# Performance work log

Measured on AMD Instinct MI355X. Metric: run time of the kernel, lower is better.

## Reference

```python
import jax, jax.numpy as jnp
import numpy as np

EPS = 1e-5
NUM_HEAD = 8
HEAD_DIM = 64
SCALE = HEAD_DIM ** -0.5


def setup_inputs() -> dict:
    key = jax.random.key(0)
    ks = jax.random.split(key, 3)
    b, n, dim = 4, 2048, 512
    inner = NUM_HEAD * HEAD_DIM  # 512
    x = jax.random.normal(ks[0], (b, n, dim), dtype=jnp.float32)
    ln_w = jnp.ones((dim,), jnp.float32)
    ln_b = jnp.zeros((dim,), jnp.float32)
    qkv_w = jax.random.normal(ks[1], (3 * inner, dim), jnp.float32) * (dim ** -0.5)
    qkv_b = jnp.zeros((3 * inner,), jnp.float32)
    out_w = jax.random.normal(ks[2], (dim, inner), jnp.float32) * (inner ** -0.5)
    out_b = jnp.zeros((dim,), jnp.float32)
    return {"x": x, "ln_w": ln_w, "ln_b": ln_b, "qkv_w": qkv_w,
            "qkv_b": qkv_b, "out_w": out_w, "out_b": out_b}


def reference(x, ln_w, ln_b, qkv_w, qkv_b, out_w, out_b):
    b, n, dim = x.shape
    # Pre-norm LayerNorm
    mu = jnp.mean(x, axis=-1, keepdims=True)
    var = jnp.mean(jnp.square(x - mu), axis=-1, keepdims=True)
    xn = (x - mu) * jax.lax.rsqrt(var + EPS) * ln_w + ln_b
    # QKV projection (torch Linear: y = x @ W.T + b)
    qkv = xn @ qkv_w.T + qkv_b  # [b, n, 3*inner]
    q, k, v = jnp.split(qkv, 3, axis=-1)
    def heads(t):  # [b, n, inner] -> [b, h, n, d]
        return t.reshape(b, n, NUM_HEAD, HEAD_DIM).transpose(0, 2, 1, 3)
    q, k, v = heads(q), heads(k), heads(v)
    # Naive full attention (materializes [b, h, n, n])
    dots = jnp.einsum('bhqd,bhkd->bhqk', q, k) * SCALE
    attn = jax.nn.softmax(dots, axis=-1)
    o = jnp.einsum('bhqk,bhkd->bhqd', attn, v)
    o = o.transpose(0, 2, 1, 3).reshape(b, n, NUM_HEAD * HEAD_DIM)
    return o @ out_w.T + out_b
```

## Files before the change

kernel.cpp:

```cpp
#include <hip/hip_runtime.h>

typedef __attribute__((ext_vector_type(8))) short bf16x8;
typedef __attribute__((ext_vector_type(4))) float floatx4;
typedef __attribute__((ext_vector_type(16))) float floatx16;
typedef __attribute__((ext_vector_type(4))) unsigned int uintx4;

#define B_    4
#define N_    2048
#define DIM_  512
#define NH_   8
#define HD_   64
#define SCALE_ 0.125f
#define SL2E_ (0.125f * 1.44269504f)

__device__ __forceinline__ unsigned short f32_to_bf16(float f) {
    return (unsigned short)((__float_as_uint(f) + 0x8000u) >> 16);
}

__device__ __forceinline__ float bf16_to_f32(unsigned short u) {
    return __uint_as_float(((unsigned int)u) << 16);
}

__device__ __forceinline__ floatx4 mfma16(bf16x8 a, bf16x8 b, floatx4 c) {
    return __builtin_amdgcn_mfma_f32_16x16x32_bf16(a, b, c, 0, 0, 0);
}

__device__ __forceinline__ floatx16 mfma32(bf16x8 a, bf16x8 b, floatx16 c) {
    return __builtin_amdgcn_mfma_f32_32x32x16_bf16(a, b, c, 0, 0, 0);
}

__device__ __forceinline__ floatx4 fzero4() {
    floatx4 z = {0.f, 0.f, 0.f, 0.f};
    return z;
}

__device__ __forceinline__ floatx16 fzero16() {
    floatx16 z;
#pragma unroll
    for (int i = 0; i < 16; i++) z[i] = 0.f;
    return z;
}

__device__ __forceinline__ unsigned int cvt_pk_bf16(float lo, float hi) {
    unsigned int r;
    asm("v_cvt_pk_bf16_f32 %0, %1, %2" : "=v"(r) : "v"(lo), "v"(hi));
    return r;
}

__device__ __forceinline__ void async16(const unsigned short* g, unsigned short* l) {
    __builtin_amdgcn_global_load_lds((const __attribute__((address_space(1))) void*)g,
                                     (__attribute__((address_space(3))) void*)l,
                                     16, 0, 0);
}

__global__ __launch_bounds__(256) void ln_cvt_kernel(const float* __restrict__ x,
                                                     const float* __restrict__ w,
                                                     const float* __restrict__ b,
                                                     unsigned short* __restrict__ xn,
                                                     const float* __restrict__ srcA,
                                                     const float* __restrict__ srcB,
                                                     unsigned short* __restrict__ dstA,
                                                     unsigned short* __restrict__ dstB) {
    const int NWQ = 3 * DIM_ * DIM_;
    if (blockIdx.x < 2048) {
        int wv = threadIdx.x >> 6;
        int lane = threadIdx.x & 63;
        int row = blockIdx.x * 4 + wv;
        const float4* xr = (const float4*)(x + (size_t)row * DIM_);
        float4 v0 = xr[lane * 2];
        float4 v1 = xr[lane * 2 + 1];
        float s  = (v0.x + v0.y + v0.z + v0.w) + (v1.x + v1.y + v1.z + v1.w);
        float sq = v0.x*v0.x + v0.y*v0.y + v0.z*v0.z + v0.w*v0.w +
                   v1.x*v1.x + v1.y*v1.y + v1.z*v1.z + v1.w*v1.w;
#pragma unroll
        for (int off = 1; off < 64; off <<= 1) {
            s  += __shfl_xor(s, off, 64);
            sq += __shfl_xor(sq, off, 64);
        }
        float mu   = s * (1.f / DIM_);
        float var  = sq * (1.f / DIM_) - mu * mu;
        float rstd = rsqrtf(var + 1e-5f);
        float4 w0 = ((const float4*)w)[lane * 2];
        float4 w1 = ((const float4*)w)[lane * 2 + 1];
        float4 b0 = ((const float4*)b)[lane * 2];
        float4 b1 = ((const float4*)b)[lane * 2 + 1];
        float y[8];
        y[0] = (v0.x - mu) * rstd * w0.x + b0.x;
        y[1] = (v0.y - mu) * rstd * w0.y + b0.y;
        y[2] = (v0.z - mu) * rstd * w0.z + b0.z;
        y[3] = (v0.w - mu) * rstd * w0.w + b0.w;
        y[4] = (v1.x - mu) * rstd * w1.x + b1.x;
        y[5] = (v1.y - mu) * rstd * w1.y + b1.y;
        y[6] = (v1.z - mu) * rstd * w1.z + b1.z;
        y[7] = (v1.w - mu) * rstd * w1.w + b1.w;
        uint4 pk;
        pk.x = (unsigned int)f32_to_bf16(y[0]) | ((unsigned int)f32_to_bf16(y[1]) << 16);
        pk.y = (unsigned int)f32_to_bf16(y[2]) | ((unsigned int)f32_to_bf16(y[3]) << 16);
        pk.z = (unsigned int)f32_to_bf16(y[4]) | ((unsigned int)f32_to_bf16(y[5]) << 16);
        pk.w = (unsigned int)f32_to_bf16(y[6]) | ((unsigned int)f32_to_bf16(y[7]) << 16);
        ((uint4*)(xn + (size_t)row * DIM_))[lane] = pk;
    } else {
        int e0 = ((blockIdx.x - 2048) * 256 + threadIdx.x) * 8;
        const float* src;
        unsigned short* dst;
        if (e0 < NWQ) { src = srcA + e0; dst = dstA + e0; }
        else          { src = srcB + (e0 - NWQ); dst = dstB + (e0 - NWQ); }
        float4 u0 = ((const float4*)src)[0];
        float4 u1 = ((const float4*)src)[1];
        uint4 pk;
        pk.x = (unsigned int)f32_to_bf16(u0.x) | ((unsigned int)f32_to_bf16(u0.y) << 16);
        pk.y = (unsigned int)f32_to_bf16(u0.z) | ((unsigned int)f32_to_bf16(u0.w) << 16);
        pk.z = (unsigned int)f32_to_bf16(u1.x) | ((unsigned int)f32_to_bf16(u1.y) << 16);
        pk.w = (unsigned int)f32_to_bf16(u1.z) | ((unsigned int)f32_to_bf16(u1.w) << 16);
        *(uint4*)dst = pk;
    }
}

#define GEMM_CORE512(A_, B_ptr, am0, bn0)                                           \
    __shared__ unsigned short Alds[2][128][32];                                     \
    __shared__ unsigned short Blds[2][128][32];                                     \
    int tid = threadIdx.x, lane = tid & 63, wid = tid >> 6;                         \
    int l15 = lane & 15, quad = lane >> 4;                                          \
    int wmloc = (wid >> 1) * 32, wnloc = (wid & 1) * 64;                            \
    int sr = lane >> 2;                                                             \
    int sc = (lane & 3) * 8;                                                        \
    int srow0 = 16 * wid;                                                           \
    floatx4 acc[2][4];                                                              \
    _Pragma("unroll")                                                               \
    for (int i = 0; i < 2; i++)                                                     \
        _Pragma("unroll")                                                           \
        for (int j = 0; j < 4; j++) acc[i][j] = fzero4();                           \
    int buf = 0;                                                                    \
    async16(A_ + (size_t)(am0 + srow0 + sr) * DIM_ + sc, &Alds[0][srow0][0]);       \
    async16(B_ptr + (size_t)(bn0 + srow0 + sr) * DIM_ + sc, &Blds[0][srow0][0]);    \
    __syncthreads();                                                                \
    for (int t = 0; t < 16; t++) {                                                  \
        if (t < 15) {                                                               \
            int k0 = (t + 1) * 32;                                                  \
            async16(A_ + (size_t)(am0 + srow0 + sr) * DIM_ + k0 + sc,               \
                    &Alds[buf ^ 1][srow0][0]);                                      \
            async16(B_ptr + (size_t)(bn0 + srow0 + sr) * DIM_ + k0 + sc,            \
                    &Blds[buf ^ 1][srow0][0]);                                      \
        }                                                                           \
        bf16x8 av[2], bv[4];                                                        \
        _Pragma("unroll")                                                           \
        for (int i = 0; i < 2; i++)                                                 \
            av[i] = *(const bf16x8*)(&Alds[buf][wmloc + 16 * i + l15][quad * 8]);   \
        _Pragma("unroll")                                                           \
        for (int j = 0; j < 4; j++)                                                 \
            bv[j] = *(const bf16x8*)(&Blds[buf][wnloc + 16 * j + l15][quad * 8]);   \
        _Pragma("unroll")                                                           \
        for (int i = 0; i < 2; i++)                                                 \
            _Pragma("unroll")                                                       \
            for (int j = 0; j < 4; j++)                                             \
                acc[i][j] = mfma16(av[i], bv[j], acc[i][j]);                        \
        __syncthreads();                                                            \
        buf ^= 1;                                                                   \
    }

__global__ __launch_bounds__(512, 6) void qkv_gemm(const unsigned short* __restrict__ A,
                                                   const unsigned short* __restrict__ Bw,
                                                   const float* __restrict__ bias,
                                                   unsigned short* __restrict__ Qh,
                                                   unsigned short* __restrict__ Kh,
                                                   unsigned short* __restrict__ Vt) {
    int am0 = blockIdx.x * 128, bn0 = blockIdx.y * 128;
    GEMM_CORE512(A, Bw, am0, bn0)

    if (bn0 >= 1024) {
        unsigned short* sc_ = &Alds[0][0][0] + wid * (16 * 40);
        int m0 = am0 + wmloc;
        int bidx = m0 >> 11;
        int t0 = m0 & 2047;
#pragma unroll
        for (int j = 0; j < 4; j++) {
            float bias_n = bias[bn0 + wnloc + 16 * j + l15];
#pragma unroll
            for (int i = 0; i < 2; i++)
#pragma unroll
                for (int r = 0; r < 4; r++)
                    sc_[l15 * 40 + 16 * i + quad * 4 + r] =
                        f32_to_bf16(acc[i][j][r] + bias_n);
            int nr = lane >> 2;
            int rem = (bn0 - 1024) + wnloc + 16 * j + nr;
            int head = rem >> 6, d = rem & 63;
            bf16x8 vv = *(const bf16x8*)(sc_ + nr * 40 + (lane & 3) * 8);
            *(bf16x8*)(Vt + ((size_t)(bidx * NH_ + head) * HD_ + d) * N_ +
                       t0 + (lane & 3) * 8) = vv;
        }
    } else {
#pragma unroll
        for (int i = 0; i < 2; i++) {
#pragma unroll
            for (int j = 0; j < 4; j++) {
                int n = bn0 + wnloc + 16 * j + l15;
                float bias_n = bias[n];
                int which = n >> 9;
                int rem = n & 511;
                int head = rem >> 6;
                int d = rem & 63;
#pragma unroll
                for (int r = 0; r < 4; r++) {
                    int m = am0 + wmloc + 16 * i + quad * 4 + r;
                    int b = m >> 11;
                    int t = m & 2047;
                    float val = acc[i][j][r] + bias_n;
                    if (which == 0) {
                        Qh[((size_t)(b * NH_ + head) * N_ + t) * HD_ + d] =
                            f32_to_bf16(val * SL2E_);
                    } else {
                        Kh[((size_t)(b * NH_ + head) * N_ + t) * HD_ + d] =
                            f32_to_bf16(val);
                    }
                }
            }
        }
    }
}

__global__ __launch_bounds__(256, 4) void out_gemm_fused(const unsigned short* __restrict__ Opart,
                                                         const float* __restrict__ lpart,
                                                         const unsigned short* __restrict__ Bw,
                                                         const float* __restrict__ bias,
                                                         float* __restrict__ out) {
    __shared__ unsigned short Alds[2][64][36];
    __shared__ unsigned short Blds[2][128][32];
    int tid = threadIdx.x, lane = tid & 63, wid = tid >> 6;
    int l15 = lane & 15, quad = lane >> 4;
    int wmloc = (wid >> 1) * 32, wnloc = (wid & 1) * 64;
    int am0 = blockIdx.x * 64, bn0 = blockIdx.y * 128;

    int arow = tid >> 2;
    int ac8 = (tid & 3) * 8;
    int token = am0 + arow;
    int bb = token >> 11;
    const size_t LSTR = (size_t)B_ * NH_ * N_;
    const size_t OSTR = (size_t)B_ * N_ * DIM_;
    const unsigned short* arow0 = Opart + (size_t)token * DIM_;
    const unsigned short* arow1 = arow0 + OSTR;

    int sr = lane >> 2;
    int sc = (lane & 3) * 8;

    floatx4 acc[2][4];
#pragma unroll
    for (int i = 0; i < 2; i++)
#pragma unroll
        for (int j = 0; j < 4; j++) acc[i][j] = fzero4();

#define STAGE_A(BUF, T)                                                         \
    {                                                                           \
        int k0 = (T) * 32;                                                      \
        int head = k0 >> 6;                                                     \
        size_t li = (size_t)(bb * NH_ + head) * N_ + (token & 2047);            \
        float l1 = lpart[li];                                                   \
        float l2 = lpart[LSTR + li];                                            \
        float inv = 1.f / (l1 + l2);                                            \
        float w1 = l1 * inv, w2 = l2 * inv;                                     \
        bf16x8 o0 = *(const bf16x8*)(arow0 + k0 + ac8);                         \
        bf16x8 o1 = *(const bf16x8*)(arow1 + k0 + ac8);                         \
        bf16x8 pk;                                                              \
        _Pragma("unroll")                                                       \
        for (int e = 0; e < 8; e++)                                             \
            pk[e] = (short)f32_to_bf16(                                         \
                w1 * bf16_to_f32((unsigned short)o0[e]) +                       \
                w2 * bf16_to_f32((unsigned short)o1[e]));                       \
        *(bf16x8*)(&Alds[BUF][arow][ac8]) = pk;                                 \
    }

#define STAGE_B(BUF, T)                                                         \
    {                                                                           \
        int k0 = (T) * 32;                                                      \
        _Pragma("unroll")                                                       \
        for (int i = 0; i < 2; i++) {                                           \
            int r0 = 32 * wid + 16 * i;                                         \
            async16(Bw + (size_t)(bn0 + r0 + sr) * DIM_ + k0 + sc,              \
                    &Blds[BUF][r0][0]);                                         \
        }                                                                       \
    }

    STAGE_B(0, 0)
    STAGE_A(0, 0)
    __syncthreads();
    int buf = 0;
    for (int t = 0; t < 16; t++) {
        if (t < 15) {
            STAGE_B(buf ^ 1, t + 1)
            STAGE_A(buf ^ 1, t + 1)
        }
        bf16x8 av[2], bv[4];
#pragma unroll
        for (int i = 0; i < 2; i++)
            av[i] = *(const bf16x8*)(&Alds[buf][wmloc + 16 * i + l15][quad * 8]);
#pragma unroll
        for (int j = 0; j < 4; j++)
            bv[j] = *(const bf16x8*)(&Blds[buf][wnloc + 16 * j + l15][quad * 8]);
#pragma unroll
        for (int i = 0; i < 2; i++)
#pragma unroll
            for (int j = 0; j < 4; j++)
                acc[i][j] = mfma16(av[i], bv[j], acc[i][j]);
        __syncthreads();
        buf ^= 1;
    }
#undef STAGE_A
#undef STAGE_B

#pragma unroll
    for (int i = 0; i < 2; i++) {
#pragma unroll
        for (int j = 0; j < 4; j++) {
            int n = bn0 + wnloc + 16 * j + l15;
            float bias_n = bias[n];
#pragma unroll
            for (int r = 0; r < 4; r++) {
                int m = am0 + wmloc + 16 * i + quad * 4 + r;
                out[(size_t)m * DIM_ + n] = acc[i][j][r] + bias_n;
            }
        }
    }
}

__global__ __launch_bounds__(512, 4) void attn_kernel(const unsigned short* __restrict__ Qh,
                                                      const unsigned short* __restrict__ Kh,
                                                      const unsigned short* __restrict__ Vtg,
                                                      unsigned short* __restrict__ Opart,
                                                      float* __restrict__ lpart) {
    int bh = blockIdx.y;
    int b = bh >> 3, head = bh & 7;
    int qt = blockIdx.x;
    int split = blockIdx.z;
    int kv0 = split << 10;
    int tid = threadIdx.x, lane = tid & 63, w = tid >> 6;
    int l31 = lane & 31, hi = lane >> 5;
    int xr = l31 & 7;

    const unsigned short* Qp = Qh + (size_t)bh * N_ * HD_;
    const unsigned short* Kg = Kh + (size_t)bh * N_ * HD_;
    const unsigned short* Vg = Vtg + (size_t)bh * HD_ * N_;

    int q0 = qt * 256 + w * 32;

    bf16x8 aQ[4];
    {
        const unsigned short* qrow = Qp + (size_t)(q0 + l31) * HD_ + hi * 8;
#pragma unroll
        for (int t = 0; t < 4; t++)
            aQ[t] = *(const bf16x8*)(qrow + 16 * t);
    }

    __shared__ unsigned short KV[4][2][64][64];
    __shared__ float l_sm[8][32];

    int srow = lane >> 3;
    int scol = ((lane & 7) ^ srow) * 8;

    const char* ptc[4];
#pragma unroll
    for (int t = 0; t < 4; t++)
        ptc[t] = (const char*)&KV[0][0][l31][(((2 * t + hi) ^ xr) * 8)];

    const unsigned short* kSrc = Kg + (size_t)(kv0 + 8 * w + srow) * HD_ + scol;
    const unsigned short* vSrc = Vg + (size_t)(8 * w + srow) * N_ + kv0 + scol;

#define STAGE_KV(BUF, IT)                                                       \
    {                                                                           \
        async16(kSrc + (size_t)(IT) * 64 * HD_, &KV[BUF][0][8 * w][0]);         \
        async16(vSrc + (size_t)(IT) * 64, &KV[BUF][1][8 * w][0]);               \
    }

#define VMW(N)  asm volatile("s_waitcnt vmcnt(" #N ")" ::: "memory")
#define RBAR()  asm volatile("s_barrier" ::: "memory")

    floatx16 of[2];
    of[0] = fzero16();
    of[1] = fzero16();
    float lsA = 0.f, lsB = 0.f;

#define COMPUTE(BUF)                                                            \
    {                                                                           \
        bf16x8 pa[4];                                                           \
        _Pragma("unroll")                                                       \
        for (int tau = 0; tau < 2; tau++) {                                     \
            bf16x8 kf[4];                                                       \
            _Pragma("unroll")                                                   \
            for (int t = 0; t < 4; t++)                                         \
                kf[t] = *(const bf16x8*)(ptc[t] + (BUF) * 16384 + tau * 4096);  \
            floatx16 acc = fzero16();                                           \
            __builtin_amdgcn_s_setprio(1);                                      \
            _Pragma("unroll")                                                   \
            for (int t = 0; t < 4; t++)                                         \
                acc = mfma32(kf[t], aQ[t], acc);                                \
            __builtin_amdgcn_s_setprio(0);                                      \
            float p[16];                                                        \
            _Pragma("unroll")                                                   \
            for (int r = 0; r < 16; r += 2) {                                   \
                p[r]     = __builtin_amdgcn_exp2f(acc[r]);                      \
                p[r + 1] = __builtin_amdgcn_exp2f(acc[r + 1]);                  \
                lsA += p[r];                                                    \
                lsB += p[r + 1];                                                \
            }                                                                   \
            unsigned int a0 = cvt_pk_bf16(p[0], p[1]);                          \
            unsigned int b0 = cvt_pk_bf16(p[4], p[5]);                          \
            unsigned int a1 = cvt_pk_bf16(p[2], p[3]);                          \
            unsigned int b1 = cvt_pk_bf16(p[6], p[7]);                          \
            unsigned int a2 = cvt_pk_bf16(p[8], p[9]);                          \
            unsigned int b2 = cvt_pk_bf16(p[12], p[13]);                        \
            unsigned int a3 = cvt_pk_bf16(p[10], p[11]);                        \
            unsigned int b3 = cvt_pk_bf16(p[14], p[15]);                        \
            asm("v_permlane32_swap_b32 %0, %1" : "+v"(a0), "+v"(b0));           \
            asm("v_permlane32_swap_b32 %0, %1" : "+v"(a1), "+v"(b1));           \
            asm("v_permlane32_swap_b32 %0, %1" : "+v"(a2), "+v"(b2));           \
            asm("v_permlane32_swap_b32 %0, %1" : "+v"(a3), "+v"(b3));           \
            uintx4 f0 = {a0, a1, b0, b1};                                       \
            uintx4 f1 = {a2, a3, b2, b3};                                       \
            pa[2 * tau]     = __builtin_bit_cast(bf16x8, f0);                   \
            pa[2 * tau + 1] = __builtin_bit_cast(bf16x8, f1);                   \
        }                                                                       \
        __builtin_amdgcn_s_setprio(1);                                          \
        _Pragma("unroll")                                                       \
        for (int s = 0; s < 4; s++) {                                           \
            _Pragma("unroll")                                                   \
            for (int dt = 0; dt < 2; dt++) {                                    \
                bf16x8 vf = *(const bf16x8*)(ptc[s] + (BUF) * 16384 + 8192 +    \
                                             dt * 4096);                        \
                of[dt] = mfma32(pa[s], vf, of[dt]);                             \
            }                                                                   \
        }                                                                       \
        __builtin_amdgcn_s_setprio(0);                                          \
    }

#define ITER(BUF, VN, SBUF, STILE, DOSTAGE)                                     \
    VMW(VN);                                                                    \
    RBAR();                                                                     \
    __builtin_amdgcn_sched_barrier(0);                                          \
    COMPUTE(BUF)                                                                \
    RBAR();                                                                     \
    if (DOSTAGE) STAGE_KV(SBUF, STILE)

    STAGE_KV(0, 0)
    STAGE_KV(1, 1)
    STAGE_KV(2, 2)

    for (int g = 0; g < 3; g++) {
        int base = g * 4;
        ITER(0, 4, 3, base + 3, 1);
        ITER(1, 4, 0, base + 4, 1);
        ITER(2, 4, 1, base + 5, 1);
        ITER(3, 4, 2, base + 6, 1);
    }
    ITER(0, 4, 3, 15, 1);
    ITER(1, 4, 0, 0, 0);
    ITER(2, 2, 0, 0, 0);
    ITER(3, 0, 0, 0, 0);
#undef ITER
#undef STAGE_KV
#undef COMPUTE
#undef VMW
#undef RBAR

    float lsum = lsA + lsB;
    lsum += __shfl_xor(lsum, 32, 64);
    if (hi == 0) {
        l_sm[w][l31] = __builtin_amdgcn_rcpf(lsum);
        lpart[(size_t)split * B_ * NH_ * N_ + (size_t)bh * N_ + q0 + l31] = lsum;
    }
    asm volatile("s_waitcnt lgkmcnt(0)" ::: "memory");

    unsigned short* Od = Opart + (size_t)split * B_ * N_ * DIM_;
#pragma unroll
    for (int r = 0; r < 16; r++) {
        int qr = (r & 3) + 8 * (r >> 2) + 4 * hi;
        float inv = l_sm[w][qr];
        int token = q0 + qr;
        size_t base = ((size_t)b * N_ + token) * DIM_ + (size_t)head * HD_;
#pragma unroll
        for (int dt = 0; dt < 2; dt++)
            Od[base + 32 * dt + l31] = f32_to_bf16(of[dt][r] * inv);
    }
}

extern "C" void kernel_launch(void* const* d_in, const int* in_sizes, int n_in,
                              void* d_out, int out_size, void* d_ws, size_t ws_size,
                              hipStream_t stream) {
    const float* x     = (const float*)d_in[0];
    const float* ln_w  = (const float*)d_in[1];
    const float* ln_b  = (const float*)d_in[2];
    const float* qkv_w = (const float*)d_in[3];
    const float* qkv_b = (const float*)d_in[4];
    const float* out_w = (const float*)d_in[5];
    const float* out_b = (const float*)d_in[6];
    float* out = (float*)d_out;

    char* ws = (char*)d_ws;
    const size_t TOK = (size_t)B_ * N_;
    unsigned short* xn    = (unsigned short*)ws;  ws += TOK * DIM_ * 2;
    unsigned short* wq_bf = (unsigned short*)ws;  ws += (size_t)3 * DIM_ * DIM_ * 2;
    unsigned short* wo_bf = (unsigned short*)ws;  ws += (size_t)DIM_ * DIM_ * 2;
    unsigned short* Qh    = (unsigned short*)ws;  ws += TOK * DIM_ * 2;
    unsigned short* Kh    = (unsigned short*)ws;  ws += TOK * DIM_ * 2;
    unsigned short* Vt    = (unsigned short*)ws;  ws += TOK * DIM_ * 2;
    unsigned short* Opart = (unsigned short*)ws;  ws += (size_t)2 * TOK * DIM_ * 2;
    float*          lpart = (float*)ws;           ws += (size_t)2 * B_ * NH_ * N_ * 4;

    ln_cvt_kernel<<<2048 + 512, 256, 0, stream>>>(x, ln_w, ln_b, xn,
                                                  qkv_w, out_w, wq_bf, wo_bf);
    qkv_gemm<<<dim3(TOK / 128, (3 * DIM_) / 128), 512, 0, stream>>>(xn, wq_bf, qkv_b, Qh, Kh, Vt);
    attn_kernel<<<dim3(N_ / 256, B_ * NH_, 2), 512, 0, stream>>>(Qh, Kh, Vt, Opart, lpart);
    out_gemm_fused<<<dim3(TOK / 64, DIM_ / 128), 256, 0, stream>>>(Opart, lpart, wo_bf, out_b, out);
}
```

Baseline: 154.7 us.

## Software-pipeline QK softmax of next tile with PV of previous tile

Restructures the attention inner loop so the QK^T plus exp for tile i+1 is interleaved with the PV MFMAs for tile i, using a prologue and an epilogue. It also drops the second barrier per iteration and reissues async staging right after each fused step, with adjusted vmcnt waits. The aim is to overlap exp/convert VALU work with matrix ops and cut sync overhead. The cost is extra live registers for the panew fragments, and correct buffer reuse now rests on a single barrier per iteration.

```diff
diff --git a/kernel.cpp b/kernel.cpp
--- a/kernel.cpp
+++ b/kernel.cpp
@@ -376,86 +376,114 @@
     of[0] = fzero16();
     of[1] = fzero16();
     float lsA = 0.f, lsB = 0.f;
-
-#define COMPUTE(BUF)                                                            \
-    {                                                                           \
-        bf16x8 pa[4];                                                           \
+    bf16x8 pa[4];
+
+#define QKSM_TAU(QB, TAU)                                                       \
+    {                                                                           \
+        bf16x8 kf0 = *(const bf16x8*)(ptc[0] + (QB) * 16384 + (TAU) * 4096);    \
+        bf16x8 kf1 = *(const bf16x8*)(ptc[1] + (QB) * 16384 + (TAU) * 4096);    \
+        bf16x8 kf2 = *(const bf16x8*)(ptc[2] + (QB) * 16384 + (TAU) * 4096);    \
+        bf16x8 kf3 = *(const bf16x8*)(ptc[3] + (QB) * 16384 + (TAU) * 4096);    \
+        floatx16 acc = fzero16();                                               \
+        __builtin_amdgcn_s_setprio(1);                                          \
+        acc = mfma32(kf0, aQ[0], acc);                                          \
+        acc = mfma32(kf1, aQ[1], acc);                                          \
+        acc = mfma32(kf2, aQ[2], acc);                                          \
+        acc = mfma32(kf3, aQ[3], acc);                                          \
+        __builtin_amdgcn_s_setprio(0);                                          \
+        float p[16];                                                            \
         _Pragma("unroll")                                                       \
-        for (int tau = 0; tau < 2; tau++) {                                     \
-            bf16x8 kf[4];                                                       \
-            _Pragma("unroll")                                                   \
-            for (int t = 0; t < 4; t++)                                         \
-                kf[t] = *(const bf16x8*)(ptc[t] + (BUF) * 16384 + tau * 4096);  \
-            floatx16 acc = fzero16();                                           \
-            __builtin_amdgcn_s_setprio(1);                                      \
-            _Pragma("unroll")                                                   \
-            for (int t = 0; t < 4; t++)                                         \
-                acc = mfma32(kf[t], aQ[t], acc);                                \
-            __builtin_amdgcn_s_setprio(0);                                      \
-            float p[16];                                                        \
-            _Pragma("unroll")                                                   \
-            for (int r = 0; r < 16; r += 2) {                                   \
-                p[r]     = __builtin_amdgcn_exp2f(acc[r]);                      \
-                p[r + 1] = __builtin_amdgcn_exp2f(acc[r + 1]);                  \
-                lsA += p[r];                                                    \
-                lsB += p[r + 1];                                                \
-            }                                                                   \
-            unsigned int a0 = cvt_pk_bf16(p[0], p[1]);                          \
-            unsigned int b0 = cvt_pk_bf16(p[4], p[5]);                          \
-            unsigned int a1 = cvt_pk_bf16(p[2], p[3]);                          \
-            unsigned int b1 = cvt_pk_bf16(p[6], p[7]);                          \
-            unsigned int a2 = cvt_pk_bf16(p[8], p[9]);                          \
-            unsigned int b2 = cvt_pk_bf16(p[12], p[13]);                        \
-            unsigned int a3 = cvt_pk_bf16(p[10], p[11]);                        \
-            unsigned int b3 = cvt_pk_bf16(p[14], p[15]);                        \
-            asm("v_permlane32_swap_b32 %0, %1" : "+v"(a0), "+v"(b0));           \
-            asm("v_permlane32_swap_b32 %0, %1" : "+v"(a1), "+v"(b1));           \
-            asm("v_permlane32_swap_b32 %0, %1" : "+v"(a2), "+v"(b2));           \
-            asm("v_permlane32_swap_b32 %0, %1" : "+v"(a3), "+v"(b3));           \
-            uintx4 f0 = {a0, a1, b0, b1};                                       \
-            uintx4 f1 = {a2, a3, b2, b3};                                       \
-            pa[2 * tau]     = __builtin_bit_cast(bf16x8, f0);                   \
-            pa[2 * tau + 1] = __builtin_bit_cast(bf16x8, f1);                   \
+        for (int r = 0; r < 16; r += 2) {                                       \
+            p[r]     = __builtin_amdgcn_exp2f(acc[r]);                          \
+            p[r + 1] = __builtin_amdgcn_exp2f(acc[r + 1]);                      \
+            lsA += p[r];                                                        \
+            lsB += p[r + 1];                                                    \
         }                                                                       \
+        unsigned int a0 = cvt_pk_bf16(p[0], p[1]);                              \
+        unsigned int b0 = cvt_pk_bf16(p[4], p[5]);                              \
+        unsigned int a1 = cvt_pk_bf16(p[2], p[3]);                              \
+        unsigned int b1 = cvt_pk_bf16(p[6], p[7]);                              \
+        unsigned int a2 = cvt_pk_bf16(p[8], p[9]);                              \
+        unsigned int b2 = cvt_pk_bf16(p[12], p[13]);                            \
+        unsigned int a3 = cvt_pk_bf16(p[10], p[11]);                            \
+        unsigned int b3 = cvt_pk_bf16(p[14], p[15]);                            \
+        asm("v_permlane32_swap_b32 %0, %1" : "+v"(a0), "+v"(b0));               \
+        asm("v_permlane32_swap_b32 %0, %1" : "+v"(a1), "+v"(b1));               \
+        asm("v_permlane32_swap_b32 %0, %1" : "+v"(a2), "+v"(b2));               \
+        asm("v_permlane32_swap_b32 %0, %1" : "+v"(a3), "+v"(b3));               \
+        uintx4 f0 = {a0, a1, b0, b1};                                           \
+        uintx4 f1 = {a2, a3, b2, b3};                                           \
+        panew[2 * (TAU)]     = __builtin_bit_cast(bf16x8, f0);                  \
+        panew[2 * (TAU) + 1] = __builtin_bit_cast(bf16x8, f1);                  \
+    }
+
+#define PVPAIR(PB, S)                                                           \
+    {                                                                           \
+        _Pragma("unroll")                                                       \
+        for (int dt = 0; dt < 2; dt++) {                                        \
+            bf16x8 vf = *(const bf16x8*)(ptc[S] + (PB) * 16384 + 8192 +         \
+                                         dt * 4096);                            \
+            of[dt] = mfma32(pa[S], vf, of[dt]);                                 \
+        }                                                                       \
+    }
+
+#define FUSED(QB, PB)                                                           \
+    {                                                                           \
+        bf16x8 panew[4];                                                        \
+        QKSM_TAU(QB, 0)                                                         \
         __builtin_amdgcn_s_setprio(1);                                          \
-        _Pragma("unroll")                                                       \
-        for (int s = 0; s < 4; s++) {                                           \
-            _Pragma("unroll")                                                   \
-            for (int dt = 0; dt < 2; dt++) {                                    \
-                bf16x8 vf = *(const bf16x8*)(ptc[s] + (BUF) * 16384 + 8192 +    \
-                                             dt * 4096);                        \
-                of[dt] = mfma32(pa[s], vf, of[dt]);                             \
-            }                                                                   \
-        }                                                                       \
+        PVPAIR(PB, 0) PVPAIR(PB, 1)                                             \
         __builtin_amdgcn_s_setprio(0);                                          \
-    }
-
-#define ITER(BUF, VN, SBUF, STILE, DOSTAGE)                                     \
+        QKSM_TAU(QB, 1)                                                         \
+        __builtin_amdgcn_s_setprio(1);                                          \
+        PVPAIR(PB, 2) PVPAIR(PB, 3)                                             \
+        __builtin_amdgcn_s_setprio(0);                                          \
+        pa[0] = panew[0]; pa[1] = panew[1];                                     \
+        pa[2] = panew[2]; pa[3] = panew[3];                                     \
+    }
+
+#define QKFIRST(QB)                                                             \
+    {                                                                           \
+        bf16x8 panew[4];                                                        \
+        QKSM_TAU(QB, 0)                                                         \
+        QKSM_TAU(QB, 1)                                                         \
+        pa[0] = panew[0]; pa[1] = panew[1];                                     \
+        pa[2] = panew[2]; pa[3] = panew[3];                                     \
+    }
+
+#define ITER(QB, PB, VN)                                                        \
     VMW(VN);                                                                    \
     RBAR();                                                                     \
     __builtin_amdgcn_sched_barrier(0);                                          \
-    COMPUTE(BUF)                                                                \
-    RBAR();                                                                     \
-    if (DOSTAGE) STAGE_KV(SBUF, STILE)
+    FUSED(QB, PB)
 
     STAGE_KV(0, 0)
     STAGE_KV(1, 1)
     STAGE_KV(2, 2)
+    VMW(4);
+    RBAR();
+    __builtin_amdgcn_sched_barrier(0);
+    QKFIRST(0)
 
     for (int g = 0; g < 3; g++) {
-        int base = g * 4;
-        ITER(0, 4, 3, base + 3, 1);
-        ITER(1, 4, 0, base + 4, 1);
-        ITER(2, 4, 1, base + 5, 1);
-        ITER(3, 4, 2, base + 6, 1);
-    }
-    ITER(0, 4, 3, 15, 1);
-    ITER(1, 4, 0, 0, 0);
-    ITER(2, 2, 0, 0, 0);
-    ITER(3, 0, 0, 0, 0);
+        int t3 = g * 4 + 3;
+        ITER(1, 0, 2); STAGE_KV(3, t3);
+        ITER(2, 1, 2); STAGE_KV(0, t3 + 1);
+        ITER(3, 2, 2); STAGE_KV(1, t3 + 2);
+        ITER(0, 3, 2); STAGE_KV(2, t3 + 3);
+    }
+    ITER(1, 0, 2); STAGE_KV(3, 15);
+    ITER(2, 1, 2);
+    ITER(3, 2, 0);
+    __builtin_amdgcn_s_setprio(1);
+    PVPAIR(3, 0) PVPAIR(3, 1) PVPAIR(3, 2) PVPAIR(3, 3)
+    __builtin_amdgcn_s_setprio(0);
 #undef ITER
+#undef QKFIRST
+#undef FUSED
+#undef PVPAIR
+#undef QKSM_TAU
 #undef STAGE_KV
-#undef COMPUTE
 #undef VMW
 #undef RBAR
 
```

Result: slower. 165.4 us (+6.9%).
